# Kernel optimization log

Hardware: AMD Instinct MI355X
Metric: run time of the kernel (lower is better)

Reference implementation:

```python
import jax, jax.numpy as jnp
import numpy as np

B, S, D = 4, 4096, 1024


def setup_inputs() -> dict:
    key = jax.random.key(0)
    ks = jax.random.split(key, 7)
    scale = 1.0 / np.sqrt(D)
    return {
        "x": jax.random.normal(ks[0], (B, S, D), dtype=jnp.float32),
        "W_in": jax.random.normal(ks[1], (D, D), dtype=jnp.float32) * scale,
        "W_select": jax.random.normal(ks[2], (D, D), dtype=jnp.float32) * scale,
        "W_gate": jax.random.normal(ks[3], (D, D), dtype=jnp.float32) * scale,
        "W_out": jax.random.normal(ks[4], (D, D), dtype=jnp.float32) * scale,
        "W_delta": jax.random.normal(ks[5], (D, D), dtype=jnp.float32) * scale,
        "log_a": jax.random.normal(ks[6], (D,), dtype=jnp.float32) * 0.1,
    }


def reference(x, W_in, W_select, W_gate, W_out, W_delta, log_a):
    # diag mode of ChaosSSMCore. nn.Linear(bias=False): y = x @ W.T
    a_base = jax.nn.sigmoid(log_a).astype(x.dtype)  # [D]
    # Precompute all per-step projections in batched GEMMs: [B,S,D]
    delta = jnp.maximum(jax.nn.softplus(jnp.einsum('bsd,ed->bse', x, W_delta)), 1e-4)
    decay = jnp.exp(-delta * a_base)                                   # [B,S,D]
    update = jax.nn.sigmoid(jnp.einsum('bsd,ed->bse', x, W_select)) \
        * jnp.tanh(jnp.einsum('bsd,ed->bse', x, W_in))                 # [B,S,D]
    gate = jax.nn.sigmoid(jnp.einsum('bsd,ed->bse', x, W_gate))        # [B,S,D]

    def step(state, inputs):
        dec_t, upd_t = inputs
        state = dec_t * state + upd_t
        return state, state

    init = jnp.zeros((x.shape[0], x.shape[2]), dtype=x.dtype)
    # scan over seq axis: move to [S,B,D]
    _, states = jax.lax.scan(step, init, (decay.transpose(1, 0, 2), update.transpose(1, 0, 2)))
    states = states.transpose(1, 0, 2)  # [B,S,D]
    out = gate * states
    y = jnp.einsum('bsd,ed->bse', out, W_out)
    return y
```

## Files before the change

kernel.cpp:

```cpp
#include <hip/hip_runtime.h>
#include <hip/hip_bf16.h>
#include <math.h>

#define B_   4
#define S_   4096
#define D_   1024
#define M_   (B_*S_)
#define NCAT (4*D_)
#define KD   1024

#define NCHUNK 128
#define CHLEN  (S_/NCHUNK)

typedef __bf16 bf16x8 __attribute__((ext_vector_type(8)));
typedef float  f32x4  __attribute__((ext_vector_type(4)));
typedef ushort ushort8v __attribute__((ext_vector_type(8)));

__device__ __forceinline__ ushort sbf(float f) {
  return __builtin_bit_cast(ushort, (__bf16)f);
}
__device__ __forceinline__ uint pk2bf(float lo, float hi) {
  return (uint)sbf(lo) | ((uint)sbf(hi) << 16);
}
__device__ __forceinline__ float bf2f(uint bits16) {
  union { uint u; float f; } v; v.u = bits16 << 16;
  return v.f;
}
__device__ __forceinline__ float frcp(float x) { return __builtin_amdgcn_rcpf(x); }

#define GLL(g, l) __builtin_amdgcn_global_load_lds( \
  (const __attribute__((address_space(1))) uint32_t*)(uintptr_t)(g), \
  (__attribute__((address_space(3))) uint32_t*)(uint32_t)(uintptr_t)(l), 16, 0, 0)

#define MFMA_(a, b, c) __builtin_amdgcn_mfma_f32_16x16x32_bf16(a, b, c, 0, 0, 0)

__global__ void k_cvt_f2b4(const float* __restrict__ in, ushort* __restrict__ out, int n4) {
  int i = blockIdx.x * blockDim.x + threadIdx.x;
  if (i >= n4) return;
  const float4 v = ((const float4*)in)[i];
  uint2 o;
  o.x = pk2bf(v.x, v.y);
  o.y = pk2bf(v.z, v.w);
  ((uint2*)out)[i] = o;
}

__global__ void k_build_wcat(const float* __restrict__ wdel, const float* __restrict__ wsel,
                             const float* __restrict__ win,  const float* __restrict__ wgat,
                             ushort* __restrict__ wcat) {
  int i = blockIdx.x * blockDim.x + threadIdx.x;
  int E = i * 4;
  int n   = E >> 10;
  int col = E & 1023;
  int p = (n >> 4) & 3;
  int e = ((n >> 6) << 4) + (n & 15);
  const float* src = (p == 0) ? wdel : (p == 1) ? wsel : (p == 2) ? win : wgat;
  const float4 v = *(const float4*)&src[(size_t)e * 1024 + col];
  uint2 o;
  o.x = pk2bf(v.x, v.y);
  o.y = pk2bf(v.z, v.w);
  *(uint2*)&wcat[E] = o;
}

__global__ void k_abase(const float* __restrict__ log_a, float* __restrict__ abase) {
  int i = blockIdx.x * blockDim.x + threadIdx.x;
  if (i < D_) abase[i] = frcp(1.f + __expf(-log_a[i]));
}

template<int MODE>
__global__ __launch_bounds__(512, 2) void gemm10(
    const ushort* __restrict__ Ab, const ushort* __restrict__ Bb, int nbn,
    float* __restrict__ outf,
    ushort* __restrict__ dec, ushort* __restrict__ uu, ushort* __restrict__ gat,
    const float* __restrict__ abase,
    float* __restrict__ cP, float* __restrict__ cL)
{
  __shared__ ushort lds[65536];

  const int nwg = gridDim.x;
  const int bid = blockIdx.x;
  const int nb  = (bid & 7) * (nwg >> 3) + (bid >> 3);
  const int brow = nb / nbn, bcol = nb % nbn;
  const int t = threadIdx.x, lane = t & 63, w = t >> 6;
  const int wm = w >> 2, wn = w & 3;
  const int l15 = lane & 15, lhi = lane >> 4;

  const int lr = t >> 2, cs = t & 3;
  const int csw = cs ^ ((lr >> 1) & 3);
  const int gA0 = (lr & 63) | ((lr & 64) << 1);
  const int gA1 = gA0 | 64;
  const int gB0 = (lr & 31) | ((lr & 0x60) << 1);
  const int gB1 = gB0 | 32;
  const uint vA0 = ((uint)(brow * 256 + gA0) * KD + (uint)csw * 8) * 2u;
  const uint vA1 = ((uint)(brow * 256 + gA1) * KD + (uint)csw * 8) * 2u;
  const uint vB0 = ((uint)(bcol * 256 + gB0) * KD + (uint)csw * 8) * 2u;
  const uint vB1 = ((uint)(bcol * 256 + gB1) * KD + (uint)csw * 8) * 2u;
  const char* Ab8 = (const char*)Ab;
  const char* Bb8 = (const char*)Bb;
  const int dstT = t * 8;

#define STG(PB, OPOFF, SRC8, VOFF, R, KO) do { \
    GLL((SRC8) + (VOFF) + (KO) * 2,      &lds[(PB) + (OPOFF) + (R) * 4096 + dstT]); \
    GLL((SRC8) + (VOFF) + (KO) * 2 + 64, &lds[(PB) + (OPOFF) + 8192 + (R) * 4096 + dstT]); } while (0)

  const int swp = (lhi ^ ((l15 >> 1) & 3)) * 8;
  const ushort* fA  = &lds[(wm * 64 + l15) * 32 + swp];
  const ushort* fB  = &lds[16384 + (wn * 32 + l15) * 32 + swp];

#define RD_A4(DST, PB, HOFF, KK) \
    _Pragma("unroll") for (int m = 0; m < 4; ++m) \
      DST[m][KK] = *(const bf16x8*)&fA[(PB) + (KK) * 8192 + (HOFF) + m * 512];
#define RD_B4(DST, PB, HOFF) \
    _Pragma("unroll") for (int n = 0; n < 2; ++n) \
    _Pragma("unroll") for (int kk = 0; kk < 2; ++kk) \
      DST[n][kk] = *(const bf16x8*)&fB[(PB) + kk * 8192 + (HOFF) + n * 512];
#define MM4(AR, BV, M0, N0) \
    _Pragma("unroll") for (int kk = 0; kk < 2; ++kk) \
    _Pragma("unroll") for (int m = 0; m < 4; ++m) \
    _Pragma("unroll") for (int n = 0; n < 2; ++n) \
      acc[(M0) + m][(N0) + n] = MFMA_(AR[m][kk], BV[n][kk], acc[(M0) + m][(N0) + n]);
#define BAR   __builtin_amdgcn_s_barrier()
#define PRIO1 __builtin_amdgcn_s_setprio(1)
#define PRIO0 __builtin_amdgcn_s_setprio(0)

  f32x4 acc[8][4] = {};
  bf16x8 a03[4][2], a47[4][2], b23[2][2], b01a[2][2], b01b[2][2];

#define KTILE(P, Q, KO, BU, BN) do { \
    RD_A4(a03, P, 0, 1) \
    RD_B4(b23, P, 4096) \
    PRIO1; MM4(a03, BU, 0, 0) PRIO0; BAR; \
    RD_A4(a47, P, 4096, 0) \
    STG(P, 16384, Bb8, vB0, 0, KO); \
    PRIO1; MM4(a03, b23, 0, 2) PRIO0; BAR; \
    RD_A4(a47, P, 4096, 1) \
    STG(P, 0, Ab8, vA0, 0, KO); \
    STG(P, 16384, Bb8, vB1, 1, KO); \
    PRIO1; MM4(a47, b23, 4, 2) PRIO0; \
    asm volatile("s_waitcnt vmcnt(6)" ::: "memory"); \
    BAR; \
    RD_A4(a03, Q, 0, 0) \
    RD_B4(BN, Q, 0) \
    STG(P, 0, Ab8, vA1, 1, KO); \
    PRIO1; MM4(a47, BU, 4, 0) PRIO0; BAR; \
  } while (0)

  STG(0, 16384, Bb8, vB0, 0, 0);
  STG(0, 0, Ab8, vA0, 0, 0);
  STG(0, 16384, Bb8, vB1, 1, 0);
  STG(0, 0, Ab8, vA1, 1, 0);
  STG(32768, 16384, Bb8, vB0, 0, 64);
  STG(32768, 0, Ab8, vA0, 0, 64);
  STG(32768, 16384, Bb8, vB1, 1, 64);
  STG(32768, 0, Ab8, vA1, 1, 64);
  asm volatile("s_waitcnt vmcnt(8)" ::: "memory");
  BAR;
  RD_A4(a03, 0, 0, 0)
  RD_B4(b01a, 0, 0)

#pragma unroll 1
  for (int i = 0; i < 8; ++i) {
    const int t2 = 2 * i + 2, t3 = 2 * i + 3;
    const int ko2 = (t2 < 16 ? t2 : 15) * 64;
    const int ko3 = (t3 < 16 ? t3 : 15) * 64;
    KTILE(0, 32768, ko2, b01a, b01b);
    KTILE(32768, 0, ko3, b01b, b01a);
  }

  asm volatile("s_waitcnt vmcnt(0)" ::: "memory");
  __syncthreads();

  const int rowb = wm * 128;
  if constexpr (MODE == 0) {
    ushort* ldsD = lds;
    ushort* ldsU = lds + 16384;
    ushort* ldsG = lds + 32768;
    const int chl = wn * 16 + l15;
    const int chg = bcol * 64 + chl;
    const float ab = abase[chg];
    float Prun[8], Lrun[8];
#pragma unroll
    for (int mf = 0; mf < 8; ++mf) {
      const int rl0 = rowb + mf * 16 + lhi * 4;
      float P = 1.f, L = 0.f;
#pragma unroll
      for (int r = 0; r < 4; ++r) {
        const float zd = acc[mf][0][r];
        const float zs = acc[mf][1][r];
        const float zi = acc[mf][2][r];
        const float zg = acc[mf][3][r];
        float sp = fmaxf(zd, 0.f) + __logf(1.f + __expf(-fabsf(zd)));
        sp = fmaxf(sp, 1e-4f);
        const float dv = __expf(-sp * ab);
        const float sv = frcp(1.f + __expf(-zs));
        float tt = __expf(-2.f * fabsf(zi));
        float tv = (1.f - tt) * frcp(1.f + tt);
        tv = (zi < 0.f) ? -tv : tv;
        const float gv = frcp(1.f + __expf(-zg));
        const ushort dbits = sbf(dv);
        const ushort ubits = sbf(sv * tv);
        const int row = rl0 + r;
        const int idx = row * 64 + ((((chl >> 3) ^ (row & 7)) << 3) | (chl & 7));
        ldsD[idx] = dbits;
        ldsU[idx] = ubits;
        ldsG[idx] = sbf(gv);
        const float dq = bf2f(dbits), uq = bf2f(ubits);
        P *= dq;
        L = fmaf(dq, L, uq);
      }
      Prun[mf] = P; Lrun[mf] = L;
    }
    const int bq = brow >> 4;
    const int cbase = (brow & 15) * 8 + wm * 4;
#pragma unroll
    for (int j = 0; j < 4; ++j) {
      float Pe = Prun[2 * j],     Le = Lrun[2 * j];
      float Po = Prun[2 * j + 1], Lo = Lrun[2 * j + 1];
      {
        float Pn = __shfl_down(Pe, 16), Ln = __shfl_down(Le, 16);
        Pe = Pe * Pn; Le = fmaf(Pn, Le, Ln);
        float Pm = __shfl_down(Po, 16), Lm = __shfl_down(Lo, 16);
        Po = Po * Pm; Lo = fmaf(Pm, Lo, Lm);
      }
      {
        float Pn = __shfl_down(Pe, 32), Ln = __shfl_down(Le, 32);
        Pe = Pe * Pn; Le = fmaf(Pn, Le, Ln);
        float Pm = __shfl_down(Po, 32), Lm = __shfl_down(Lo, 32);
        Po = Po * Pm; Lo = fmaf(Pm, Lo, Lm);
      }
      if (lhi == 0) {
        const float Pc = Pe * Po;
        const float Lc = fmaf(Po, Le, Lo);
        const size_t o = ((size_t)(bq * NCHUNK + cbase + j)) * D_ + chg;
        cP[o] = Pc; cL[o] = Lc;
      }
    }
    __syncthreads();
    const int srow = t >> 3, cD = t & 7;
    const size_t gbase = (size_t)(brow * 256) * D_ + bcol * 64 + cD * 8;
#pragma unroll
    for (int itp = 0; itp < 4; ++itp) {
      const int row = itp * 64 + srow;
      const int lidx = row * 64 + ((cD ^ (row & 7)) << 3);
      const size_t g = gbase + (size_t)row * D_;
      *(ushort8v*)&dec[g] = *(const ushort8v*)&ldsD[lidx];
      *(ushort8v*)&uu[g]  = *(const ushort8v*)&ldsU[lidx];
      *(ushort8v*)&gat[g] = *(const ushort8v*)&ldsG[lidx];
    }
  } else {
    const int colb = bcol * 256 + wn * 64;
#pragma unroll
    for (int mf = 0; mf < 8; ++mf) {
      const int rl0 = brow * 256 + rowb + mf * 16 + lhi * 4;
#pragma unroll
      for (int nf = 0; nf < 4; ++nf) {
        const int gc = colb + nf * 16 + l15;
#pragma unroll
        for (int r = 0; r < 4; ++r)
          outf[(size_t)(rl0 + r) * 1024 + gc] = acc[mf][nf][r];
      }
    }
  }
#undef KTILE
#undef STG
#undef RD_A4
#undef RD_B4
#undef MM4
}

__global__ __launch_bounds__(64) void k_scanB(
    const float* __restrict__ cP, const float* __restrict__ cL, float* __restrict__ carry)
{
  const int idx = blockIdx.x * 64 + threadIdx.x;
  const int b = idx >> 10, e = idx & 1023;
  float st = 0.f;
  size_t base = (size_t)b * NCHUNK * D_ + e;
  for (int c = 0; c < NCHUNK; ++c) {
    size_t o = base + (size_t)c * D_;
    carry[o] = st;
    st = fmaf(cP[o], st, cL[o]);
  }
}

__global__ __launch_bounds__(512) void k_scanC(
    const ushort* __restrict__ dec, const ushort* __restrict__ uu,
    const ushort* __restrict__ gat, const float* __restrict__ carry,
    ushort* __restrict__ outb)
{
  const int t  = threadIdx.x;
  const int c  = blockIdx.x & (NCHUNK - 1);
  const int b  = blockIdx.x >> 7;
  const int e2 = t * 2;
  size_t co = ((size_t)b * NCHUNK + c) * D_ + e2;
  float s0 = carry[co], s1 = carry[co + 1];
  size_t base = ((size_t)b * S_ + (size_t)c * CHLEN) * D_ + e2;
  for (int i = 0; i < CHLEN; ++i) {
    const uint dv = *(const uint*)(dec + base);
    const uint uv = *(const uint*)(uu + base);
    const uint gv = *(const uint*)(gat + base);
    s0 = fmaf(bf2f(dv & 0xffffu), s0, bf2f(uv & 0xffffu));
    s1 = fmaf(bf2f(dv >> 16),     s1, bf2f(uv >> 16));
    float o0 = bf2f(gv & 0xffffu) * s0;
    float o1 = bf2f(gv >> 16)     * s1;
    *(uint*)(outb + base) = pk2bf(o0, o1);
    base += D_;
  }
}

extern "C" void kernel_launch(void* const* d_in, const int* in_sizes, int n_in,
                              void* d_out, int out_size, void* d_ws, size_t ws_size,
                              hipStream_t stream) {
  const float* x     = (const float*)d_in[0];
  const float* W_in  = (const float*)d_in[1];
  const float* W_sel = (const float*)d_in[2];
  const float* W_gat = (const float*)d_in[3];
  const float* W_out = (const float*)d_in[4];
  const float* W_del = (const float*)d_in[5];
  const float* log_a = (const float*)d_in[6];
  float* y = (float*)d_out;

  char* ws = (char*)d_ws;
  size_t off = 0;
  auto alloc = [&](size_t bytes) { char* p = ws + off; off += (bytes + 255) & ~(size_t)255; return p; };
  ushort* xbf   = (ushort*)alloc((size_t)M_ * D_ * 2);
  ushort* wcat  = (ushort*)alloc((size_t)NCAT * D_ * 2);
  ushort* woutb = (ushort*)alloc((size_t)D_ * D_ * 2);
  ushort* dec   = (ushort*)alloc((size_t)M_ * D_ * 2);
  ushort* uu    = (ushort*)alloc((size_t)M_ * D_ * 2);
  ushort* gat   = (ushort*)alloc((size_t)M_ * D_ * 2);
  float*  cP    = (float*)alloc((size_t)B_ * NCHUNK * D_ * 4);
  float*  cL    = (float*)alloc((size_t)B_ * NCHUNK * D_ * 4);
  float*  carry = (float*)alloc((size_t)B_ * NCHUNK * D_ * 4);
  float*  abase = (float*)alloc(D_ * 4);
  ushort* outb  = xbf;

  k_cvt_f2b4<<<(M_ * D_ / 4 + 255) / 256, 256, 0, stream>>>(x, xbf, M_ * D_ / 4);
  k_build_wcat<<<(NCAT * D_ / 4 + 255) / 256, 256, 0, stream>>>(W_del, W_sel, W_in, W_gat, wcat);
  k_cvt_f2b4<<<(D_ * D_ / 4 + 255) / 256, 256, 0, stream>>>(W_out, woutb, D_ * D_ / 4);
  k_abase<<<(D_ + 255) / 256, 256, 0, stream>>>(log_a, abase);

  gemm10<0><<<(M_ / 256) * (NCAT / 256), 512, 0, stream>>>(
      xbf, wcat, NCAT / 256, nullptr, dec, uu, gat, abase, cP, cL);

  k_scanB<<<(B_ * D_) / 64, 64, 0, stream>>>(cP, cL, carry);
  k_scanC<<<B_ * NCHUNK, 512, 0, stream>>>(dec, uu, gat, carry, outb);

  gemm10<1><<<(M_ / 256) * (D_ / 256), 512, 0, stream>>>(
      outb, woutb, D_ / 256, y, nullptr, nullptr, nullptr, nullptr, nullptr, nullptr);
}
```

Baseline: 256.7 us.

## Merge prep kernels, inline abase, fold carry scan into chunk scan

The three conversion kernels and the abase kernel are merged into one prep launch, and sigmoid(log_a) is computed inline in the first GEMM epilogue. The separate serial carry-scan kernel is removed. Each chunk block of k_scanC now recomputes its incoming carry by walking all prior chunk summaries itself. This cuts launch count and the serial 128-step scanB kernel. In exchange, later chunks do redundant O(c) reads of cP/cL, which is quadratic total work, though small relative to the data.

New measurement: 270.3 us. 5.3% more time.

```diff
diff --git a/kernel.cpp b/kernel.cpp
--- a/kernel.cpp
+++ b/kernel.cpp
@@ -34,36 +34,38 @@
 
 #define MFMA_(a, b, c) __builtin_amdgcn_mfma_f32_16x16x32_bf16(a, b, c, 0, 0, 0)
 
-__global__ void k_cvt_f2b4(const float* __restrict__ in, ushort* __restrict__ out, int n4) {
+#define NQ_X  (M_*D_/4)
+#define NQ_W  (NCAT*D_/4)
+#define NQ_O  (D_*D_/4)
+__global__ void k_prep(const float* __restrict__ x,
+                       const float* __restrict__ wdel, const float* __restrict__ wsel,
+                       const float* __restrict__ win,  const float* __restrict__ wgat,
+                       const float* __restrict__ wout,
+                       ushort* __restrict__ xbf, ushort* __restrict__ wcat,
+                       ushort* __restrict__ woutb) {
   int i = blockIdx.x * blockDim.x + threadIdx.x;
-  if (i >= n4) return;
-  const float4 v = ((const float4*)in)[i];
+  const float* src;
+  ushort* dst;
+  size_t so, eo;
+  if (i < NQ_X) {
+    src = x; dst = xbf; so = (size_t)i * 4; eo = so;
+  } else if (i < NQ_X + NQ_W) {
+    const int q = i - NQ_X;
+    const int E = q * 4;
+    const int n = E >> 10, col = E & 1023;
+    const int p = (n >> 4) & 3;
+    const int e = ((n >> 6) << 4) + (n & 15);
+    src = (p == 0) ? wdel : (p == 1) ? wsel : (p == 2) ? win : wgat;
+    dst = wcat; so = (size_t)e * 1024 + col; eo = E;
+  } else if (i < NQ_X + NQ_W + NQ_O) {
+    const int q = i - NQ_X - NQ_W;
+    src = wout; dst = woutb; so = (size_t)q * 4; eo = so;
+  } else return;
+  const float4 v = *(const float4*)&src[so];
   uint2 o;
   o.x = pk2bf(v.x, v.y);
   o.y = pk2bf(v.z, v.w);
-  ((uint2*)out)[i] = o;
-}
-
-__global__ void k_build_wcat(const float* __restrict__ wdel, const float* __restrict__ wsel,
-                             const float* __restrict__ win,  const float* __restrict__ wgat,
-                             ushort* __restrict__ wcat) {
-  int i = blockIdx.x * blockDim.x + threadIdx.x;
-  int E = i * 4;
-  int n   = E >> 10;
-  int col = E & 1023;
-  int p = (n >> 4) & 3;
-  int e = ((n >> 6) << 4) + (n & 15);
-  const float* src = (p == 0) ? wdel : (p == 1) ? wsel : (p == 2) ? win : wgat;
-  const float4 v = *(const float4*)&src[(size_t)e * 1024 + col];
-  uint2 o;
-  o.x = pk2bf(v.x, v.y);
-  o.y = pk2bf(v.z, v.w);
-  *(uint2*)&wcat[E] = o;
-}
-
-__global__ void k_abase(const float* __restrict__ log_a, float* __restrict__ abase) {
-  int i = blockIdx.x * blockDim.x + threadIdx.x;
-  if (i < D_) abase[i] = frcp(1.f + __expf(-log_a[i]));
+  *(uint2*)&dst[eo] = o;
 }
 
 template<int MODE>
@@ -71,7 +73,7 @@
     const ushort* __restrict__ Ab, const ushort* __restrict__ Bb, int nbn,
     float* __restrict__ outf,
     ushort* __restrict__ dec, ushort* __restrict__ uu, ushort* __restrict__ gat,
-    const float* __restrict__ abase,
+    const float* __restrict__ log_a,
     float* __restrict__ cP, float* __restrict__ cL)
 {
   __shared__ ushort lds[65536];
@@ -176,7 +178,7 @@
     ushort* ldsG = lds + 32768;
     const int chl = wn * 16 + l15;
     const int chg = bcol * 64 + chl;
-    const float ab = abase[chg];
+    const float ab = frcp(1.f + __expf(-log_a[chg]));
     float Prun[8], Lrun[8];
 #pragma unroll
     for (int mf = 0; mf < 8; ++mf) {
@@ -267,31 +269,27 @@
 #undef MM4
 }
 
-__global__ __launch_bounds__(64) void k_scanB(
-    const float* __restrict__ cP, const float* __restrict__ cL, float* __restrict__ carry)
-{
-  const int idx = blockIdx.x * 64 + threadIdx.x;
-  const int b = idx >> 10, e = idx & 1023;
-  float st = 0.f;
-  size_t base = (size_t)b * NCHUNK * D_ + e;
-  for (int c = 0; c < NCHUNK; ++c) {
-    size_t o = base + (size_t)c * D_;
-    carry[o] = st;
-    st = fmaf(cP[o], st, cL[o]);
-  }
-}
-
 __global__ __launch_bounds__(512) void k_scanC(
     const ushort* __restrict__ dec, const ushort* __restrict__ uu,
-    const ushort* __restrict__ gat, const float* __restrict__ carry,
+    const ushort* __restrict__ gat,
+    const float* __restrict__ cP, const float* __restrict__ cL,
     ushort* __restrict__ outb)
 {
   const int t  = threadIdx.x;
   const int c  = blockIdx.x & (NCHUNK - 1);
   const int b  = blockIdx.x >> 7;
   const int e2 = t * 2;
-  size_t co = ((size_t)b * NCHUNK + c) * D_ + e2;
-  float s0 = carry[co], s1 = carry[co + 1];
+  float s0 = 0.f, s1 = 0.f;
+  {
+    size_t pb = (size_t)b * NCHUNK * D_ + e2;
+    for (int j = 0; j < c; ++j) {
+      const size_t o = pb + (size_t)j * D_;
+      const float2 p = *(const float2*)&cP[o];
+      const float2 l = *(const float2*)&cL[o];
+      s0 = fmaf(p.x, s0, l.x);
+      s1 = fmaf(p.y, s1, l.y);
+    }
+  }
   size_t base = ((size_t)b * S_ + (size_t)c * CHLEN) * D_ + e2;
   for (int i = 0; i < CHLEN; ++i) {
     const uint dv = *(const uint*)(dec + base);
@@ -329,20 +327,16 @@
   ushort* gat   = (ushort*)alloc((size_t)M_ * D_ * 2);
   float*  cP    = (float*)alloc((size_t)B_ * NCHUNK * D_ * 4);
   float*  cL    = (float*)alloc((size_t)B_ * NCHUNK * D_ * 4);
-  float*  carry = (float*)alloc((size_t)B_ * NCHUNK * D_ * 4);
-  float*  abase = (float*)alloc(D_ * 4);
   ushort* outb  = xbf;
 
-  k_cvt_f2b4<<<(M_ * D_ / 4 + 255) / 256, 256, 0, stream>>>(x, xbf, M_ * D_ / 4);
-  k_build_wcat<<<(NCAT * D_ / 4 + 255) / 256, 256, 0, stream>>>(W_del, W_sel, W_in, W_gat, wcat);
-  k_cvt_f2b4<<<(D_ * D_ / 4 + 255) / 256, 256, 0, stream>>>(W_out, woutb, D_ * D_ / 4);
-  k_abase<<<(D_ + 255) / 256, 256, 0, stream>>>(log_a, abase);
+  const int nq = NQ_X + NQ_W + NQ_O;
+  k_prep<<<(nq + 255) / 256, 256, 0, stream>>>(
+      x, W_del, W_sel, W_in, W_gat, W_out, xbf, wcat, woutb);
 
   gemm10<0><<<(M_ / 256) * (NCAT / 256), 512, 0, stream>>>(
-      xbf, wcat, NCAT / 256, nullptr, dec, uu, gat, abase, cP, cL);
-
-  k_scanB<<<(B_ * D_) / 64, 64, 0, stream>>>(cP, cL, carry);
-  k_scanC<<<B_ * NCHUNK, 512, 0, stream>>>(dec, uu, gat, carry, outb);
+      xbf, wcat, NCAT / 256, nullptr, dec, uu, gat, log_a, cP, cL);
+
+  k_scanC<<<B_ * NCHUNK, 512, 0, stream>>>(dec, uu, gat, cP, cL, outb);
 
   gemm10<1><<<(M_ / 256) * (D_ / 256), 512, 0, stream>>>(
       outb, woutb, D_ / 256, y, nullptr, nullptr, nullptr, nullptr, nullptr, nullptr);
```
